# Optimization experiments

Hardware: AMD Instinct MI355X
Metric: run time of the kernel (lower is better)

Reference implementation:

```python
import jax, jax.numpy as jnp
import numpy as np

N_NODES = 50000
N_EDGES = 800000
C_IN = 64
C_HID = 64
C_OUT = 64


def _glorot(key, shape):
    lim = (6.0 / (shape[0] + shape[1])) ** 0.5
    return jax.random.uniform(key, shape, jnp.float32, -lim, lim)


def setup_inputs() -> dict:
    key = jax.random.key(0)
    ks = jax.random.split(key, 8)
    x = jax.random.normal(ks[0], (N_NODES, C_IN), jnp.float32)
    edge_index = jax.random.randint(ks[1], (2, N_EDGES), 0, N_NODES, jnp.int64)
    return {
        "x": x,
        "edge_index": edge_index,
        # ChebConv layer 1 (K=2): lins[0], lins[1], bias
        "W1_0": _glorot(ks[2], (C_IN, C_HID)),
        "W1_1": _glorot(ks[3], (C_IN, C_HID)),
        "b1": jnp.zeros((C_HID,), jnp.float32),
        # ChebConv layer 2 (K=2)
        "W2_0": _glorot(ks[4], (C_HID, C_OUT)),
        "W2_1": _glorot(ks[5], (C_HID, C_OUT)),
        "b2": jnp.zeros((C_OUT,), jnp.float32),
    }


def _lhat_matvec(x, src, dst, num_nodes):
    """Apply scaled Laplacian L_hat = -D^{-1/2} A D^{-1/2} (PyG ChebConv,
    sym norm, lambda_max=2; diagonal cancels exactly)."""
    ones = jnp.ones(src.shape[0], x.dtype)
    deg = jnp.zeros(num_nodes, x.dtype).at[src].add(ones)
    dis = jnp.where(deg > 0, deg ** -0.5, 0.0)  # deg_inv_sqrt, inf -> 0
    w = -(dis[src] * dis[dst])                  # per-edge weight
    # gather source features, scale, scatter-add to destinations
    return jnp.zeros_like(x).at[dst].add(w[:, None] * x[src])


def reference(x, edge_index, W1_0, W1_1, b1, W2_0, W2_1, b2):
    src, dst = edge_index[0], edge_index[1]
    n = x.shape[0]
    # ChebConv 1: T0 = x, T1 = L_hat x
    h = x @ W1_0 + _lhat_matvec(x, src, dst, n) @ W1_1 + b1
    h = jax.nn.relu(h)
    # ChebConv 2
    out = h @ W2_0 + _lhat_matvec(h, src, dst, n) @ W2_1 + b2
    return out
```

## Files before the change

### kernel.cpp

```cpp
#include <hip/hip_runtime.h>
#include <hip/hip_bf16.h>

#define NN 50000
#define NE 800000
#define C  64
#define CAP 56
#define NTILE (NN / 16)
#define HW 12500
#define EB 128
#define EC (NE / EB)

typedef __attribute__((ext_vector_type(4))) float f32x4;
typedef __attribute__((ext_vector_type(8))) short s16x8;

__device__ __forceinline__ float ldv(const void* p, int i, int mode) {
    return mode ? __bfloat162float(((const __hip_bfloat16*)p)[i])
                : ((const float*)p)[i];
}
__device__ __forceinline__ float bflo(unsigned u) { return __uint_as_float(u << 16); }
__device__ __forceinline__ float bfhi(unsigned u) { return __uint_as_float(u & 0xffff0000u); }
__device__ __forceinline__ unsigned f2bf(float f) {
    __hip_bfloat16 h = __float2bfloat16(f);
    return (unsigned)*reinterpret_cast<unsigned short*>(&h);
}
__device__ __forceinline__ int detect_i64(const int* __restrict__ ei) {
    int z = 0;
#pragma unroll
    for (int k = 0; k < 8; ++k) z += (ei[2 * k + 1] == 0);
    return z == 8;
}
__device__ __forceinline__ int detect_bf16(const unsigned* __restrict__ xw) {
    int hits = 0;
#pragma unroll
    for (int k = 0; k < 16; ++k) {
        unsigned hb = (xw[k] >> 8) & 0x7Fu;
        hits += (hb >= 0x37u && hb <= 0x41u);
    }
    return hits >= 8;
}

__device__ __forceinline__ void lded2(const int* __restrict__ ei, int e, int i64,
                                      int& s0, int& s1, int& d0, int& d1) {
    if (i64) {
        int4 sv = *(const int4*)(ei + 2 * e);
        int4 dv = *(const int4*)(ei + 2 * (NE + e));
        s0 = sv.x; s1 = sv.z; d0 = dv.x; d1 = dv.z;
    } else {
        int2 sv = *(const int2*)(ei + e);
        int2 dv = *(const int2*)(ei + NE + e);
        s0 = sv.x; s1 = sv.y; d0 = dv.x; d1 = dv.y;
    }
}

__global__ void __launch_bounds__(1024) hist_kernel(const int* __restrict__ ei,
                                                    unsigned* __restrict__ srcp,
                                                    unsigned* __restrict__ dstp) {
    extern __shared__ unsigned sh[];
    int t = threadIdx.x;
    for (int i = t; i < 2 * HW; i += 1024) sh[i] = 0u;
    __syncthreads();
    int i64 = detect_i64(ei);
    int base = blockIdx.x * EC;
    for (int p = t; p < EC / 2; p += 1024) {
        int e = base + 2 * p;
        int s0, s1, d0, d1;
        lded2(ei, e, i64, s0, s1, d0, d1);
        atomicAdd(&sh[s0 >> 2], 1u << (8 * (s0 & 3)));
        atomicAdd(&sh[s1 >> 2], 1u << (8 * (s1 & 3)));
        atomicAdd(&sh[HW + (d0 >> 2)], 1u << (8 * (d0 & 3)));
        atomicAdd(&sh[HW + (d1 >> 2)], 1u << (8 * (d1 & 3)));
    }
    __syncthreads();
    unsigned* so = srcp + blockIdx.x * HW;
    unsigned* dd = dstp + blockIdx.x * HW;
    for (int i = t; i < HW; i += 1024) { so[i] = sh[i]; dd[i] = sh[HW + i]; }
}

__global__ void offs_kernel(const unsigned* __restrict__ srcp, unsigned* __restrict__ dstp,
                            float* __restrict__ dis, unsigned* __restrict__ pcnt) {
    int t = blockIdx.x * blockDim.x + threadIdx.x;
    if (t < HW) {
        unsigned c0 = 0, c1 = 0, c2 = 0, c3 = 0;
        for (int b = 0; b < EB; ++b) {
            unsigned v = srcp[b * HW + t];
            c0 += v & 255u; c1 += (v >> 8) & 255u; c2 += (v >> 16) & 255u; c3 += v >> 24;
        }
        float4 o;
        o.x = c0 ? rsqrtf((float)c0) : 0.f;
        o.y = c1 ? rsqrtf((float)c1) : 0.f;
        o.z = c2 ? rsqrtf((float)c2) : 0.f;
        o.w = c3 ? rsqrtf((float)c3) : 0.f;
        ((float4*)dis)[t] = o;
    } else if (t < 2 * HW) {
        int w = t - HW;
        unsigned r0 = 0, r1 = 0, r2 = 0, r3 = 0;
        for (int b = 0; b < EB; ++b) {
            unsigned v = dstp[b * HW + w];
            dstp[b * HW + w] = r0 | (r1 << 8) | (r2 << 16) | (r3 << 24);
            r0 += v & 255u; r1 += (v >> 8) & 255u; r2 += (v >> 16) & 255u; r3 += v >> 24;
        }
        uint4 pc; pc.x = r0; pc.y = r1; pc.z = r2; pc.w = r3;
        ((uint4*)pcnt)[w] = pc;
    }
}

__global__ void __launch_bounds__(1024) build_kernel(const int* __restrict__ ei,
                                                     const unsigned* __restrict__ dstp,
                                                     const float* __restrict__ dis,
                                                     int2* __restrict__ pairs) {
    extern __shared__ unsigned sh[];
    unsigned* cnt = sh;
    unsigned* off = sh + HW;
    int t = threadIdx.x;
    const unsigned* my = dstp + blockIdx.x * HW;
    for (int i = t; i < HW; i += 1024) { cnt[i] = 0u; off[i] = my[i]; }
    __syncthreads();
    int i64 = detect_i64(ei);
    int base = blockIdx.x * EC;
    for (int p = t; p < EC / 2; p += 1024) {
        int e = base + 2 * p;
        int s0, s1, d0, d1;
        lded2(ei, e, i64, s0, s1, d0, d1);
        unsigned sh0 = 8 * (d0 & 3), sh1 = 8 * (d1 & 3);
        unsigned old0 = atomicAdd(&cnt[d0 >> 2], 1u << sh0);
        unsigned w0 = ((old0 >> sh0) & 255u) + ((off[d0 >> 2] >> sh0) & 255u);
        if (w0 < CAP) pairs[d0 * CAP + w0] = make_int2(s0, __float_as_int(dis[s0]));
        unsigned old1 = atomicAdd(&cnt[d1 >> 2], 1u << sh1);
        unsigned w1 = ((old1 >> sh1) & 255u) + ((off[d1 >> 2] >> sh1) & 255u);
        if (w1 < CAP) pairs[d1 * CAP + w1] = make_int2(s1, __float_as_int(dis[s1]));
    }
}

__global__ void conv_all(const void* __restrict__ x,
                         const void* W10, const void* W11, const void* W20, const void* W21,
                         const void* b1, const void* b2,
                         unsigned short* __restrict__ xb,
                         __hip_bfloat16* __restrict__ wbf, float* __restrict__ biasf) {
    int m = detect_bf16((const unsigned*)x);
    int b = blockIdx.x, t = threadIdx.x;
    if (b < NN * C / 4 / 256) {
        int i4 = b * 256 + t;
        if (m) {
            ((uint2*)xb)[i4] = ((const uint2*)x)[i4];
        } else {
            float4 v = ((const float4*)x)[i4];
            uint2 o;
            o.x = (f2bf(v.y) << 16) | f2bf(v.x);
            o.y = (f2bf(v.w) << 16) | f2bf(v.z);
            ((uint2*)xb)[i4] = o;
        }
    } else if (b < NN * C / 4 / 256 + 4) {
        int wi = b - NN * C / 4 / 256;
        const void* src = (wi == 0) ? W10 : (wi == 1) ? W11 : (wi == 2) ? W20 : W21;
        for (int i = t; i < C * C; i += 256)
            wbf[wi * C * C + i] = __float2bfloat16(ldv(src, i, m));
    } else {
        for (int i = t; i < 2 * C; i += 256)
            biasf[i] = ldv((i < C) ? b1 : b2, i & (C - 1), m);
    }
}

__device__ __forceinline__ void acc8(float* a, float w, uint4 f) {
    a[0] += w * bflo(f.x);  a[1] += w * bfhi(f.x);
    a[2] += w * bflo(f.y);  a[3] += w * bfhi(f.y);
    a[4] += w * bflo(f.z);  a[5] += w * bfhi(f.z);
    a[6] += w * bflo(f.w);  a[7] += w * bfhi(f.w);
}
__global__ void gather_kernel(const unsigned short* __restrict__ xb,
                              unsigned short* __restrict__ y,
                              const unsigned* __restrict__ pcnt,
                              const int2* __restrict__ pairs,
                              const float* __restrict__ dis) {
    int wave = threadIdx.x >> 6, lane = threadIdx.x & 63;
    int g = lane >> 3, l8 = lane & 7;
    int r = (blockIdx.x * 4 + wave) * 8 + g;
    if (r >= NN) return;
    unsigned n = pcnt[r];
    if (n > CAP) n = CAP;
    const int2* pp = pairs + (unsigned)r * CAP;
    float a[8];
#pragma unroll
    for (int k = 0; k < 8; ++k) a[k] = 0.f;
    for (unsigned j = 0; j < n; j += 4) {
        int4 q0 = *(const int4*)(pp + j);
        int4 q1 = *(const int4*)(pp + j + 2);
        int   s0 = q0.x, s1 = q0.z, s2 = q1.x, s3 = q1.z;
        float w0 = __int_as_float(q0.y), w1 = __int_as_float(q0.w);
        float w2 = __int_as_float(q1.y), w3 = __int_as_float(q1.w);
        if (j + 1 >= n) { s1 = 0; w1 = 0.f; }
        if (j + 2 >= n) { s2 = 0; w2 = 0.f; }
        if (j + 3 >= n) { s3 = 0; w3 = 0.f; }
        uint4 f0 = *(const uint4*)(xb + s0 * C + l8 * 8);
        uint4 f1 = *(const uint4*)(xb + s1 * C + l8 * 8);
        uint4 f2 = *(const uint4*)(xb + s2 * C + l8 * 8);
        uint4 f3 = *(const uint4*)(xb + s3 * C + l8 * 8);
        acc8(a, w0, f0); acc8(a, w1, f1); acc8(a, w2, f2); acc8(a, w3, f3);
    }
    float sc = -dis[r];
    uint4 o;
    o.x = (f2bf(a[1] * sc) << 16) | f2bf(a[0] * sc);
    o.y = (f2bf(a[3] * sc) << 16) | f2bf(a[2] * sc);
    o.z = (f2bf(a[5] * sc) << 16) | f2bf(a[4] * sc);
    o.w = (f2bf(a[7] * sc) << 16) | f2bf(a[6] * sc);
    *(uint4*)(y + r * C + l8 * 8) = o;
}

template <bool RELU>
__global__ void gemm_kernel(const __hip_bfloat16* __restrict__ xb,
                            const __hip_bfloat16* __restrict__ y,
                            const __hip_bfloat16* __restrict__ wb,
                            const float* __restrict__ biasf,
                            void* __restrict__ out,
                            const unsigned* __restrict__ xorig) {
    int wave = threadIdx.x >> 6, lane = threadIdx.x & 63;
    int q = lane >> 4, n15 = lane & 15;
    const short* W0 = (const short*)wb;
    const short* W1 = (const short*)(wb + C * C);
    int out_bf16 = detect_bf16(xorig);

    s16x8 bf[4][4];
    for (int c = 0; c < 4; ++c)
        for (int t = 0; t < 4; ++t) {
            const short* W = (t < 2) ? W0 : W1;
            int rowbase = (t & 1) * 32 + q * 8;
            s16x8 v;
#pragma unroll
            for (int j = 0; j < 8; ++j) v[j] = W[(rowbase + j) * C + c * 16 + n15];
            bf[c][t] = v;
        }
    float bias0[4];
    for (int c = 0; c < 4; ++c) bias0[c] = biasf[c * 16 + n15];

    for (int tile = blockIdx.x * 4 + wave; tile < NTILE; tile += gridDim.x * 4) {
        int nb = tile * 16;
        f32x4 acc[4];
#pragma unroll
        for (int c = 0; c < 4; ++c) acc[c] = (f32x4){0.f, 0.f, 0.f, 0.f};
#pragma unroll
        for (int t = 0; t < 4; ++t) {
            const short* src = (t < 2) ? (const short*)xb : (const short*)y;
            s16x8 a = *(const s16x8*)(src + (nb + n15) * C + (t & 1) * 32 + q * 8);
#pragma unroll
            for (int c = 0; c < 4; ++c)
                acc[c] = __builtin_amdgcn_mfma_f32_16x16x32_bf16(a, bf[c][t], acc[c], 0, 0, 0);
        }
        if (out_bf16) {
            __hip_bfloat16* o = (__hip_bfloat16*)out;
#pragma unroll
            for (int c = 0; c < 4; ++c)
#pragma unroll
                for (int i = 0; i < 4; ++i) {
                    float v = acc[c][i] + bias0[c];
                    if (RELU) v = fmaxf(v, 0.f);
                    o[(nb + q * 4 + i) * C + c * 16 + n15] = __float2bfloat16(v);
                }
        } else {
            float* o = (float*)out;
#pragma unroll
            for (int c = 0; c < 4; ++c)
#pragma unroll
                for (int i = 0; i < 4; ++i) {
                    float v = acc[c][i] + bias0[c];
                    if (RELU) v = fmaxf(v, 0.f);
                    o[(nb + q * 4 + i) * C + c * 16 + n15] = v;
                }
        }
    }
}

template <bool RELU>
__global__ void gemm_kernel_bf16out(const __hip_bfloat16* __restrict__ xb,
                                    const __hip_bfloat16* __restrict__ y,
                                    const __hip_bfloat16* __restrict__ wb,
                                    const float* __restrict__ biasf,
                                    __hip_bfloat16* __restrict__ o) {
    int wave = threadIdx.x >> 6, lane = threadIdx.x & 63;
    int q = lane >> 4, n15 = lane & 15;
    const short* W0 = (const short*)wb;
    const short* W1 = (const short*)(wb + C * C);
    s16x8 bf[4][4];
    for (int c = 0; c < 4; ++c)
        for (int t = 0; t < 4; ++t) {
            const short* W = (t < 2) ? W0 : W1;
            int rowbase = (t & 1) * 32 + q * 8;
            s16x8 v;
#pragma unroll
            for (int j = 0; j < 8; ++j) v[j] = W[(rowbase + j) * C + c * 16 + n15];
            bf[c][t] = v;
        }
    float bias0[4];
    for (int c = 0; c < 4; ++c) bias0[c] = biasf[c * 16 + n15];

    for (int tile = blockIdx.x * 4 + wave; tile < NTILE; tile += gridDim.x * 4) {
        int nb = tile * 16;
        f32x4 acc[4];
#pragma unroll
        for (int c = 0; c < 4; ++c) acc[c] = (f32x4){0.f, 0.f, 0.f, 0.f};
#pragma unroll
        for (int t = 0; t < 4; ++t) {
            const short* src = (t < 2) ? (const short*)xb : (const short*)y;
            s16x8 a = *(const s16x8*)(src + (nb + n15) * C + (t & 1) * 32 + q * 8);
#pragma unroll
            for (int c = 0; c < 4; ++c)
                acc[c] = __builtin_amdgcn_mfma_f32_16x16x32_bf16(a, bf[c][t], acc[c], 0, 0, 0);
        }
#pragma unroll
        for (int c = 0; c < 4; ++c)
#pragma unroll
            for (int i = 0; i < 4; ++i) {
                float v = acc[c][i] + bias0[c];
                if (RELU) v = fmaxf(v, 0.f);
                o[(nb + q * 4 + i) * C + c * 16 + n15] = __float2bfloat16(v);
            }
    }
}

extern "C" void kernel_launch(void* const* d_in, const int* in_sizes, int n_in,
                              void* d_out, int out_size, void* d_ws, size_t ws_size,
                              hipStream_t stream) {
    const void* x    = d_in[0];
    const int*  ei   = (const int*)d_in[1];
    const void* W1_0 = d_in[2];
    const void* W1_1 = d_in[3];
    const void* b1   = d_in[4];
    const void* W2_0 = d_in[5];
    const void* W2_1 = d_in[6];
    const void* b2   = d_in[7];

    char* ws = (char*)d_ws;
    float*    dis   = (float*)(ws + 4096);
    unsigned* pcnt  = (unsigned*)(ws + 208896);
    float*    biasf = (float*)(ws + 413696);
    __hip_bfloat16* wbf = (__hip_bfloat16*)(ws + 414208);
    int2*     pairs = (int2*)(ws + 450560);
    unsigned short* xb = (unsigned short*)(ws + 22851584);
    unsigned short* y  = (unsigned short*)(ws + 29251584);
    __hip_bfloat16* h  = (__hip_bfloat16*)(ws + 35651584);
    unsigned* srcp  = (unsigned*)(ws + 42051584);
    unsigned* dstp  = (unsigned*)(ws + 48451584);

    hist_kernel<<<EB, 1024, 2 * HW * 4, stream>>>(ei, srcp, dstp);
    offs_kernel<<<(2 * HW + 255) / 256, 256, 0, stream>>>(srcp, dstp, dis, pcnt);
    build_kernel<<<EB, 1024, 2 * HW * 4, stream>>>(ei, dstp, dis, pairs);

    conv_all<<<NN * C / 4 / 256 + 5, 256, 0, stream>>>(x, W1_0, W1_1, W2_0, W2_1, b1, b2,
                                                       xb, wbf, biasf);

    gather_kernel<<<(NN + 31) / 32, 256, 0, stream>>>(xb, y, pcnt, pairs, dis);
    gemm_kernel_bf16out<true><<<782, 256, 0, stream>>>((const __hip_bfloat16*)xb,
                                                       (const __hip_bfloat16*)y, wbf, biasf, h);

    gather_kernel<<<(NN + 31) / 32, 256, 0, stream>>>((const unsigned short*)h, y, pcnt, pairs, dis);
    gemm_kernel<false><<<782, 256, 0, stream>>>(h, (const __hip_bfloat16*)y,
                                                wbf + 2 * C * C, biasf + C, d_out,
                                                (const unsigned*)x);
}
```

Before: 188.0 us.

## Pack edge pairs to 32 bits, fuse histogram with conversion, parallelize offsets

```diff
diff --git a/kernel.cpp b/kernel.cpp
--- a/kernel.cpp
+++ b/kernel.cpp
@@ -9,6 +9,8 @@
 #define HW 12500
 #define EB 128
 #define EC (NE / EB)
+#define QB (EB / 4)
+#define CONVB 782
 
 typedef __attribute__((ext_vector_type(4))) float f32x4;
 typedef __attribute__((ext_vector_type(8))) short s16x8;
@@ -52,62 +54,116 @@
     }
 }
 
-__global__ void __launch_bounds__(1024) hist_kernel(const int* __restrict__ ei,
-                                                    unsigned* __restrict__ srcp,
-                                                    unsigned* __restrict__ dstp) {
+__global__ void __launch_bounds__(1024) histconv_kernel(
+        const int* __restrict__ ei, const void* __restrict__ x,
+        const void* W10, const void* W11, const void* W20, const void* W21,
+        const void* b1, const void* b2,
+        unsigned* __restrict__ srcp, unsigned* __restrict__ dstp,
+        unsigned short* __restrict__ xb,
+        __hip_bfloat16* __restrict__ wbf, float* __restrict__ biasf) {
     extern __shared__ unsigned sh[];
-    int t = threadIdx.x;
-    for (int i = t; i < 2 * HW; i += 1024) sh[i] = 0u;
-    __syncthreads();
-    int i64 = detect_i64(ei);
-    int base = blockIdx.x * EC;
-    for (int p = t; p < EC / 2; p += 1024) {
-        int e = base + 2 * p;
-        int s0, s1, d0, d1;
-        lded2(ei, e, i64, s0, s1, d0, d1);
-        atomicAdd(&sh[s0 >> 2], 1u << (8 * (s0 & 3)));
-        atomicAdd(&sh[s1 >> 2], 1u << (8 * (s1 & 3)));
-        atomicAdd(&sh[HW + (d0 >> 2)], 1u << (8 * (d0 & 3)));
-        atomicAdd(&sh[HW + (d1 >> 2)], 1u << (8 * (d1 & 3)));
-    }
-    __syncthreads();
-    unsigned* so = srcp + blockIdx.x * HW;
-    unsigned* dd = dstp + blockIdx.x * HW;
-    for (int i = t; i < HW; i += 1024) { so[i] = sh[i]; dd[i] = sh[HW + i]; }
+    int b = blockIdx.x, t = threadIdx.x;
+    if (b < EB) {
+        for (int i = t; i < 2 * HW; i += 1024) sh[i] = 0u;
+        __syncthreads();
+        int i64 = detect_i64(ei);
+        int base = b * EC;
+        for (int p = t; p < EC / 2; p += 1024) {
+            int e = base + 2 * p;
+            int s0, s1, d0, d1;
+            lded2(ei, e, i64, s0, s1, d0, d1);
+            atomicAdd(&sh[s0 >> 2], 1u << (8 * (s0 & 3)));
+            atomicAdd(&sh[s1 >> 2], 1u << (8 * (s1 & 3)));
+            atomicAdd(&sh[HW + (d0 >> 2)], 1u << (8 * (d0 & 3)));
+            atomicAdd(&sh[HW + (d1 >> 2)], 1u << (8 * (d1 & 3)));
+        }
+        __syncthreads();
+        unsigned* so = srcp + b * HW;
+        unsigned* dd = dstp + b * HW;
+        for (int i = t; i < HW; i += 1024) { so[i] = sh[i]; dd[i] = sh[HW + i]; }
+    } else if (b < EB + CONVB) {
+        int m = detect_bf16((const unsigned*)x);
+        int i4 = (b - EB) * 1024 + t;
+        if (i4 < NN * C / 4) {
+            if (m) {
+                ((uint2*)xb)[i4] = ((const uint2*)x)[i4];
+            } else {
+                float4 v = ((const float4*)x)[i4];
+                uint2 o;
+                o.x = (f2bf(v.y) << 16) | f2bf(v.x);
+                o.y = (f2bf(v.w) << 16) | f2bf(v.z);
+                ((uint2*)xb)[i4] = o;
+            }
+        }
+    } else if (b < EB + CONVB + 4) {
+        int m = detect_bf16((const unsigned*)x);
+        int wi = b - EB - CONVB;
+        const void* src = (wi == 0) ? W10 : (wi == 1) ? W11 : (wi == 2) ? W20 : W21;
+        for (int i = t; i < C * C; i += 1024)
+            wbf[wi * C * C + i] = __float2bfloat16(ldv(src, i, m));
+    } else {
+        int m = detect_bf16((const unsigned*)x);
+        if (t < 2 * C) biasf[t] = ldv((t < C) ? b1 : b2, t & (C - 1), m);
+    }
 }
 
 __global__ void offs_kernel(const unsigned* __restrict__ srcp, unsigned* __restrict__ dstp,
                             float* __restrict__ dis, unsigned* __restrict__ pcnt) {
     int t = blockIdx.x * blockDim.x + threadIdx.x;
-    if (t < HW) {
+    if (t < 4 * HW) {
+        int w = t >> 2, c = t & 3;
         unsigned c0 = 0, c1 = 0, c2 = 0, c3 = 0;
-        for (int b = 0; b < EB; ++b) {
-            unsigned v = srcp[b * HW + t];
+        for (int b = c * QB; b < c * QB + QB; ++b) {
+            unsigned v = srcp[b * HW + w];
             c0 += v & 255u; c1 += (v >> 8) & 255u; c2 += (v >> 16) & 255u; c3 += v >> 24;
         }
-        float4 o;
-        o.x = c0 ? rsqrtf((float)c0) : 0.f;
-        o.y = c1 ? rsqrtf((float)c1) : 0.f;
-        o.z = c2 ? rsqrtf((float)c2) : 0.f;
-        o.w = c3 ? rsqrtf((float)c3) : 0.f;
-        ((float4*)dis)[t] = o;
-    } else if (t < 2 * HW) {
-        int w = t - HW;
-        unsigned r0 = 0, r1 = 0, r2 = 0, r3 = 0;
-        for (int b = 0; b < EB; ++b) {
+        c0 += __shfl_xor(c0, 1); c0 += __shfl_xor(c0, 2);
+        c1 += __shfl_xor(c1, 1); c1 += __shfl_xor(c1, 2);
+        c2 += __shfl_xor(c2, 1); c2 += __shfl_xor(c2, 2);
+        c3 += __shfl_xor(c3, 1); c3 += __shfl_xor(c3, 2);
+        if (c == 0) {
+            float4 o;
+            o.x = c0 ? rsqrtf((float)c0) : 0.f;
+            o.y = c1 ? rsqrtf((float)c1) : 0.f;
+            o.z = c2 ? rsqrtf((float)c2) : 0.f;
+            o.w = c3 ? rsqrtf((float)c3) : 0.f;
+            ((float4*)dis)[w] = o;
+        }
+    } else if (t < 8 * HW) {
+        int u = t - 4 * HW;
+        int w = u >> 2, c = u & 3;
+        int b0 = c * QB;
+        unsigned l0 = 0, l1 = 0, l2 = 0, l3 = 0;
+        for (int b = b0; b < b0 + QB; ++b) {
+            unsigned v = dstp[b * HW + w];
+            l0 += v & 255u; l1 += (v >> 8) & 255u; l2 += (v >> 16) & 255u; l3 += v >> 24;
+        }
+        unsigned i0 = l0, i1 = l1, i2 = l2, i3 = l3, p;
+        p = __shfl_up(i0, 1, 4); if (c >= 1) i0 += p;
+        p = __shfl_up(i0, 2, 4); if (c >= 2) i0 += p;
+        p = __shfl_up(i1, 1, 4); if (c >= 1) i1 += p;
+        p = __shfl_up(i1, 2, 4); if (c >= 2) i1 += p;
+        p = __shfl_up(i2, 1, 4); if (c >= 1) i2 += p;
+        p = __shfl_up(i2, 2, 4); if (c >= 2) i2 += p;
+        p = __shfl_up(i3, 1, 4); if (c >= 1) i3 += p;
+        p = __shfl_up(i3, 2, 4); if (c >= 2) i3 += p;
+        unsigned r0 = i0 - l0, r1 = i1 - l1, r2 = i2 - l2, r3 = i3 - l3;
+        for (int b = b0; b < b0 + QB; ++b) {
             unsigned v = dstp[b * HW + w];
             dstp[b * HW + w] = r0 | (r1 << 8) | (r2 << 16) | (r3 << 24);
             r0 += v & 255u; r1 += (v >> 8) & 255u; r2 += (v >> 16) & 255u; r3 += v >> 24;
         }
-        uint4 pc; pc.x = r0; pc.y = r1; pc.z = r2; pc.w = r3;
-        ((uint4*)pcnt)[w] = pc;
+        if (c == 3) {
+            uint4 pc; pc.x = r0; pc.y = r1; pc.z = r2; pc.w = r3;
+            ((uint4*)pcnt)[w] = pc;
+        }
     }
 }
 
 __global__ void __launch_bounds__(1024) build_kernel(const int* __restrict__ ei,
                                                      const unsigned* __restrict__ dstp,
                                                      const float* __restrict__ dis,
-                                                     int2* __restrict__ pairs) {
+                                                     unsigned* __restrict__ pairs) {
     extern __shared__ unsigned sh[];
     unsigned* cnt = sh;
     unsigned* off = sh + HW;
@@ -124,39 +180,10 @@
         unsigned sh0 = 8 * (d0 & 3), sh1 = 8 * (d1 & 3);
         unsigned old0 = atomicAdd(&cnt[d0 >> 2], 1u << sh0);
         unsigned w0 = ((old0 >> sh0) & 255u) + ((off[d0 >> 2] >> sh0) & 255u);
-        if (w0 < CAP) pairs[d0 * CAP + w0] = make_int2(s0, __float_as_int(dis[s0]));
+        if (w0 < CAP) pairs[d0 * CAP + w0] = (unsigned)s0 | (f2bf(dis[s0]) << 16);
         unsigned old1 = atomicAdd(&cnt[d1 >> 2], 1u << sh1);
         unsigned w1 = ((old1 >> sh1) & 255u) + ((off[d1 >> 2] >> sh1) & 255u);
-        if (w1 < CAP) pairs[d1 * CAP + w1] = make_int2(s1, __float_as_int(dis[s1]));
-    }
-}
-
-__global__ void conv_all(const void* __restrict__ x,
-                         const void* W10, const void* W11, const void* W20, const void* W21,
-                         const void* b1, const void* b2,
-                         unsigned short* __restrict__ xb,
-                         __hip_bfloat16* __restrict__ wbf, float* __restrict__ biasf) {
-    int m = detect_bf16((const unsigned*)x);
-    int b = blockIdx.x, t = threadIdx.x;
-    if (b < NN * C / 4 / 256) {
-        int i4 = b * 256 + t;
-        if (m) {
-            ((uint2*)xb)[i4] = ((const uint2*)x)[i4];
-        } else {
-            float4 v = ((const float4*)x)[i4];
-            uint2 o;
-            o.x = (f2bf(v.y) << 16) | f2bf(v.x);
-            o.y = (f2bf(v.w) << 16) | f2bf(v.z);
-            ((uint2*)xb)[i4] = o;
-        }
-    } else if (b < NN * C / 4 / 256 + 4) {
-        int wi = b - NN * C / 4 / 256;
-        const void* src = (wi == 0) ? W10 : (wi == 1) ? W11 : (wi == 2) ? W20 : W21;
-        for (int i = t; i < C * C; i += 256)
-            wbf[wi * C * C + i] = __float2bfloat16(ldv(src, i, m));
-    } else {
-        for (int i = t; i < 2 * C; i += 256)
-            biasf[i] = ldv((i < C) ? b1 : b2, i & (C - 1), m);
+        if (w1 < CAP) pairs[d1 * CAP + w1] = (unsigned)s1 | (f2bf(dis[s1]) << 16);
     }
 }
 
@@ -169,7 +196,7 @@
 __global__ void gather_kernel(const unsigned short* __restrict__ xb,
                               unsigned short* __restrict__ y,
                               const unsigned* __restrict__ pcnt,
-                              const int2* __restrict__ pairs,
+                              const unsigned* __restrict__ pairs,
                               const float* __restrict__ dis) {
     int wave = threadIdx.x >> 6, lane = threadIdx.x & 63;
     int g = lane >> 3, l8 = lane & 7;
@@ -177,16 +204,14 @@
     if (r >= NN) return;
     unsigned n = pcnt[r];
     if (n > CAP) n = CAP;
-    const int2* pp = pairs + (unsigned)r * CAP;
+    const unsigned* pp = pairs + (unsigned)r * CAP;
     float a[8];
 #pragma unroll
     for (int k = 0; k < 8; ++k) a[k] = 0.f;
     for (unsigned j = 0; j < n; j += 4) {
-        int4 q0 = *(const int4*)(pp + j);
-        int4 q1 = *(const int4*)(pp + j + 2);
-        int   s0 = q0.x, s1 = q0.z, s2 = q1.x, s3 = q1.z;
-        float w0 = __int_as_float(q0.y), w1 = __int_as_float(q0.w);
-        float w2 = __int_as_float(q1.y), w3 = __int_as_float(q1.w);
+        uint4 q = *(const uint4*)(pp + j);
+        int   s0 = q.x & 0xFFFF, s1 = q.y & 0xFFFF, s2 = q.z & 0xFFFF, s3 = q.w & 0xFFFF;
+        float w0 = bfhi(q.x), w1 = bfhi(q.y), w2 = bfhi(q.z), w3 = bfhi(q.w);
         if (j + 1 >= n) { s1 = 0; w1 = 0.f; }
         if (j + 2 >= n) { s2 = 0; w2 = 0.f; }
         if (j + 3 >= n) { s3 = 0; w3 = 0.f; }
@@ -332,19 +357,17 @@
     unsigned* pcnt  = (unsigned*)(ws + 208896);
     float*    biasf = (float*)(ws + 413696);
     __hip_bfloat16* wbf = (__hip_bfloat16*)(ws + 414208);
-    int2*     pairs = (int2*)(ws + 450560);
-    unsigned short* xb = (unsigned short*)(ws + 22851584);
-    unsigned short* y  = (unsigned short*)(ws + 29251584);
-    __hip_bfloat16* h  = (__hip_bfloat16*)(ws + 35651584);
-    unsigned* srcp  = (unsigned*)(ws + 42051584);
-    unsigned* dstp  = (unsigned*)(ws + 48451584);
-
-    hist_kernel<<<EB, 1024, 2 * HW * 4, stream>>>(ei, srcp, dstp);
-    offs_kernel<<<(2 * HW + 255) / 256, 256, 0, stream>>>(srcp, dstp, dis, pcnt);
+    unsigned* pairs = (unsigned*)(ws + 450560);
+    unsigned short* xb = (unsigned short*)(ws + 11651072);
+    unsigned short* y  = (unsigned short*)(ws + 18051072);
+    __hip_bfloat16* h  = (__hip_bfloat16*)(ws + 24451072);
+    unsigned* srcp  = (unsigned*)(ws + 30851072);
+    unsigned* dstp  = (unsigned*)(ws + 37251072);
+
+    histconv_kernel<<<EB + CONVB + 5, 1024, 2 * HW * 4, stream>>>(
+        ei, x, W1_0, W1_1, W2_0, W2_1, b1, b2, srcp, dstp, xb, wbf, biasf);
+    offs_kernel<<<(8 * HW + 255) / 256, 256, 0, stream>>>(srcp, dstp, dis, pcnt);
     build_kernel<<<EB, 1024, 2 * HW * 4, stream>>>(ei, dstp, dis, pairs);
-
-    conv_all<<<NN * C / 4 / 256 + 5, 256, 0, stream>>>(x, W1_0, W1_1, W2_0, W2_1, b1, b2,
-                                                       xb, wbf, biasf);
 
     gather_kernel<<<(NN + 31) / 32, 256, 0, stream>>>(xb, y, pcnt, pairs, dis);
     gemm_kernel_bf16out<true><<<782, 256, 0, stream>>>((const __hip_bfloat16*)xb,
```

Measured after the change: 172.7 us. -8.1%, faster.
